# Optimization experiments

Measured on AMD Instinct MI355X. Metric: run time of the kernel, lower is better.

Reference implementation:

```python
import jax, jax.numpy as jnp
import numpy as np

B, T1, T2, D, H = 16, 512, 64, 768, 12
E = D // H  # head dim


def _proj(x, W, b):
    # x: [B,T,D], W: [6,D,D], b: [6,D] -> [6,B,H,T,E], scaled by E**-0.25 (applied to q,k,v alike, per source)
    t = x.shape[1]
    p = jnp.einsum('btd,kdf->kbtf', x, W) + b[:, None, None, :]
    p = p.reshape(6, B, t, H, E).transpose(0, 1, 3, 2, 4)
    return p * (E ** -0.25)


def setup_inputs() -> dict:
    key = jax.random.key(0)
    ks = jax.random.split(key, 12)
    s = 0.02
    return {
        'feats': jax.random.normal(ks[0], (B, T1, D), jnp.float32),
        'inps': jax.random.normal(ks[1], (B, T2, D), jnp.float32),
        'att_mask': jax.random.randint(ks[2], (B, 1, 1, T1 + T2), 0, 2).astype(bool),
        'W_f': s * jax.random.normal(ks[3], (6, D, D), jnp.float32),
        'b_f': s * jax.random.normal(ks[4], (6, D), jnp.float32),
        'W_i': s * jax.random.normal(ks[5], (6, D, D), jnp.float32),
        'b_i': s * jax.random.normal(ks[6], (6, D), jnp.float32),
        'Wu_v': s * jax.random.normal(ks[7], (D, D), jnp.float32),
        'bu_v': s * jax.random.normal(ks[8], (D,), jnp.float32),
        'Wu_l': s * jax.random.normal(ks[9], (D, D), jnp.float32),
        'bu_l': s * jax.random.normal(ks[10], (D,), jnp.float32),
    }


def reference(feats, inps, att_mask, W_f, b_f, W_i, b_i, Wu_v, bu_v, Wu_l, bu_l):
    NEG = jnp.float32(-1e9)
    # projections from feats: [keys_v_v, queries_v_v, values_v_v, queries_l_v, keys_v_l, values_v_l]
    k_vv, q_vv, v_vv, q_lv, k_vl, v_vl = _proj(feats, W_f, b_f)
    # projections from inps: [keys_l_v, values_l_v, queries_v_l, queries_l_l, keys_l_l, values_l_l]
    k_lv, v_lv, q_vl, q_ll, k_ll, v_ll = _proj(inps, W_i, b_i)

    # visual stream: two distinct queries over the two key blocks, joint softmax over t1+t2
    dot_vv = jnp.einsum('bhqe,bhke->bhqk', q_vv, k_vv)   # [B,H,T1,T1]
    dot_lv = jnp.einsum('bhqe,bhke->bhqk', q_lv, k_lv)   # [B,H,T1,T2]
    att_v = jnp.concatenate([dot_vv, dot_lv], axis=-1)    # [B,H,T1,T1+T2]
    att_v = jax.nn.softmax(jnp.where(att_mask, NEG, att_v), axis=-1)
    vals_v = jnp.concatenate([v_vv, v_lv], axis=2)        # [B,H,T1+T2,E]
    out_v = jnp.einsum('bhqk,bhke->bhqe', att_v, vals_v)
    out_v = out_v.transpose(0, 2, 1, 3).reshape(B, T1, D)
    out_v = out_v @ Wu_v + bu_v

    # language stream
    dot_vl = jnp.einsum('bhqe,bhke->bhqk', q_vl, k_vl)    # [B,H,T2,T1]
    dot_ll = jnp.einsum('bhqe,bhke->bhqk', q_ll, k_ll)    # [B,H,T2,T2]
    att_l = jnp.concatenate([dot_vl, dot_ll], axis=-1)    # [B,H,T2,T1+T2]
    att_l = jax.nn.softmax(jnp.where(att_mask, NEG, att_l), axis=-1)
    vals_l = jnp.concatenate([v_vl, v_ll], axis=2)        # [B,H,T1+T2,E]
    out_l = jnp.einsum('bhqk,bhke->bhqe', att_l, vals_l)
    out_l = out_l.transpose(0, 2, 1, 3).reshape(B, T2, D)
    out_l = out_l @ Wu_l + bu_l

    return (out_v, out_l)
```

## Files before the change

### kernel.cpp

```cpp
#include <hip/hip_runtime.h>
#include <stdint.h>

#define BB 16
#define T1C 512
#define T2C 64
#define DC 768
#define HC 12
#define EC 64
#define SC 576
#define QSCALE 0.35355339059327379f

typedef __attribute__((ext_vector_type(8))) short bf16x8;
typedef __attribute__((ext_vector_type(4))) float f32x4;

__device__ __forceinline__ uint16_t f2b(float f) {
    union { float f; uint32_t i; } v; v.f = f;
    return (uint16_t)((v.i + 0x7fffu + ((v.i >> 16) & 1u)) >> 16);
}
__device__ __forceinline__ uint16_t f2bfast(float f) {
    union { float f; uint32_t i; } v; v.f = f;
    return (uint16_t)((v.i + 0x8000u) >> 16);
}
__device__ __forceinline__ uint32_t pk2(float a, float b) {
    return (uint32_t)f2b(a) | ((uint32_t)f2b(b) << 16);
}

__device__ __forceinline__ void gll16(const void* g, void* l) {
    __builtin_amdgcn_global_load_lds(
        (const __attribute__((address_space(1))) uint32_t*)(uintptr_t)g,
        (__attribute__((address_space(3))) uint32_t*)(uintptr_t)l, 16, 0, 0);
}

#define WT_BLOCKS (24 * 24 * 14)
#define XS_BLOCKS 3456

__global__ __launch_bounds__(256) void prep(
    const float* __restrict__ Wf, const float* __restrict__ Wi,
    const float* __restrict__ Wuv, const float* __restrict__ Wul,
    uint16_t* __restrict__ Wt,
    const float* __restrict__ Xf, const float* __restrict__ Xi,
    uint16_t* __restrict__ Of, uint16_t* __restrict__ Oi,
    const uint32_t* __restrict__ mw, int* __restrict__ flags)
{
    __shared__ union { float tile[32][33]; int d[3]; } sh;
    const int bid = blockIdx.x;
    if (bid < WT_BLOCKS) {
        const int z = bid / 576, r = bid % 576;
        const int kx = r % 24, fy = r / 24;
        const float* src = (z < 6)  ? Wf + (size_t)z * DC * DC
                         : (z < 12) ? Wi + (size_t)(z - 6) * DC * DC
                         : (z == 12 ? Wuv : Wul);
        uint16_t* dst = Wt + (size_t)z * DC * DC;
        const int tx = threadIdx.x & 31, ty = threadIdx.x >> 5;
        const int k0 = kx * 32, f0 = fy * 32;
#pragma unroll
        for (int q = 0; q < 4; q++)
            sh.tile[ty + q * 8][tx] = src[(size_t)(k0 + ty + q * 8) * DC + f0 + tx];
        __syncthreads();
#pragma unroll
        for (int q = 0; q < 4; q++)
            dst[(size_t)(f0 + ty + q * 8) * DC + k0 + tx] = f2b(sh.tile[tx][ty + q * 8]);
    } else if (bid < WT_BLOCKS + XS_BLOCKS) {
        const int nf = BB * T1C * DC / 8;
        const int ni = BB * T2C * DC / 8;
        int t = (bid - WT_BLOCKS) * 256 + threadIdx.x;
        const float* src; uint16_t* dst; int cc;
        if (t < nf) { src = Xf; dst = Of; cc = t; }
        else        { cc = t - nf; if (cc >= ni) return; src = Xi; dst = Oi; }
        int rlid = cc & 15;
        int t2 = cc >> 4;
        int qd = t2 & 3;
        int t3 = t2 >> 2;
        int kt = t3 % 24;
        int p  = t3 / 24;
        const float* sp = src + (size_t)(p * 16 + rlid) * DC + kt * 32 + qd * 8;
        float4 a = *(const float4*)sp;
        float4 b = *(const float4*)(sp + 4);
        uint4 o;
        o.x = pk2(a.x, a.y); o.y = pk2(a.z, a.w);
        o.z = pk2(b.x, b.y); o.w = pk2(b.z, b.w);
        *(uint4*)(dst + (size_t)cc * 8) = o;
    } else {
        if (threadIdx.x == 0) { sh.d[0] = 0; sh.d[1] = 0; sh.d[2] = 0; }
        __syncthreads();
        int lW = 0, lB = 0, lL = 0;
        for (int i = threadIdx.x; i < 2304; i += 256) {
            uint32_t w = mw[i];
            if (w > 1u) lW = 1;
            if (((w) & 0xffu) > 1u || ((w >> 8) & 0xffu) > 1u ||
                ((w >> 16) & 0xffu) > 1u || ((w >> 24) & 0xffu) > 1u) lB = 1;
            if ((w & 0xffffu) > 1u) lL = 1;
        }
        if (lW) atomicOr(&sh.d[0], 1);
        if (lB) atomicOr(&sh.d[1], 1);
        if (lL) atomicOr(&sh.d[2], 1);
        __syncthreads();
        if (threadIdx.x == 0)
            flags[0] = (!sh.d[0]) ? 0 : ((!sh.d[1]) ? 1 : (sh.d[2] ? 2 : 0));
    }
}

#define BSTR 76

__global__ __launch_bounds__(256, 3) void gemm_proj_mfma(
    const uint16_t* __restrict__ Xsf, const uint16_t* __restrict__ Xsi,
    const uint16_t* __restrict__ Wt,
    const float* __restrict__ b_f, const float* __restrict__ b_i,
    uint16_t* __restrict__ Pf, uint16_t* __restrict__ Pi)
{
    __shared__ union {
        uint16_t B[2][128 * 32];
        uint16_t bounce[4][16 * BSTR];
    } sm;
    const int tid = threadIdx.x;
    const int w = tid >> 6, l = tid & 63;
    const bool isf = (blockIdx.x < 64);
    const int mx = isf ? blockIdx.x : blockIdx.x - 64;
    const int m0 = mx * 128;
    const int T  = isf ? T1C : T2C;
    const uint16_t* Xs = isf ? Xsf : Xsi;
    const float* bias  = isf ? b_f : b_i;
    uint16_t* P        = isf ? Pf : Pi;
    const int vmask    = isf ? 0x24 : 0x22;
    const int k6 = blockIdx.y / 6, nt = blockIdx.y % 6;
    const int n0 = nt * 128;
    const uint16_t* Bsrc = Wt + (size_t)((isf ? 0 : 6) + k6) * DC * DC;

    const int lid = l & 15, qd = l >> 4;
    const int wm = w >> 1, wn = w & 1;
    const int br = l >> 2, bk = (l & 3) * 8;
    const int p0 = mx * 8 + wm * 4;
    const int c0 = w * 2;

    f32x4 acc[4][4] = {};
    bf16x8 af0[4], af1[4];

#define PJ_A(dst, t) { _Pragma("unroll") for (int i = 0; i < 4; i++) \
        dst[i] = *(const bf16x8*)(Xs + ((size_t)((p0 + i) * 24 + (t)) * 64 + l) * 8); }
#define PJ_S(bu, t) { _Pragma("unroll") for (int n = 0; n < 2; n++) \
        gll16(Bsrc + (size_t)(n0 + (c0 + n) * 16 + br) * DC + (t) * 32 + bk, \
              &sm.B[bu][(c0 + n) * 512]); }
#define PJ_C(bu, afc) { bf16x8 bq[4]; \
        _Pragma("unroll") for (int j = 0; j < 4; j++) \
            bq[j] = *(const bf16x8*)&sm.B[bu][(wn * 64 + j * 16 + lid) * 32 + qd * 8]; \
        _Pragma("unroll") for (int i = 0; i < 4; i++) \
        _Pragma("unroll") for (int j = 0; j < 4; j++) \
            acc[i][j] = __builtin_amdgcn_mfma_f32_16x16x32_bf16(afc[i], bq[j], acc[i][j], 0, 0, 0); }

    PJ_A(af0, 0);
    PJ_S(0, 0);

    for (int k2 = 0; k2 < 12; ++k2) {
        PJ_A(af1, 2 * k2 + 1);
        __builtin_amdgcn_s_barrier();
        __builtin_amdgcn_sched_barrier(0);
        PJ_S(1, 2 * k2 + 1);
        asm volatile("s_waitcnt vmcnt(6)" ::: "memory");
        __builtin_amdgcn_sched_barrier(0);
        __builtin_amdgcn_s_barrier();
        __builtin_amdgcn_sched_barrier(0);
        PJ_C(0, af0);
        if (k2 < 11) { PJ_A(af0, 2 * k2 + 2); }
        __builtin_amdgcn_s_barrier();
        __builtin_amdgcn_sched_barrier(0);
        if (k2 < 11) {
            PJ_S(0, 2 * k2 + 2);
            asm volatile("s_waitcnt vmcnt(6)" ::: "memory");
        } else {
            asm volatile("s_waitcnt vmcnt(0)" ::: "memory");
        }
        __builtin_amdgcn_sched_barrier(0);
        __builtin_amdgcn_s_barrier();
        __builtin_amdgcn_sched_barrier(0);
        PJ_C(1, af1);
    }
#undef PJ_A
#undef PJ_S
#undef PJ_C

    float bv[4];
#pragma unroll
    for (int j = 0; j < 4; j++)
        bv[j] = bias[k6 * DC + n0 + wn * 64 + j * 16 + lid];
    __syncthreads();

    uint16_t* reg = sm.bounce[w];
    const int mb = m0 + wm * 64;
    const int b = mb / T, tb = mb - b * T;
    const int h = nt * 2 + wn;
    const int rrow = l >> 2;
    const int rcol = (l & 3) * 16;

    if (!((vmask >> k6) & 1)) {
        uint16_t* dst0 = P + ((((size_t)k6 * BB + b) * HC + h) * T + tb + rrow) * EC + rcol;
#pragma unroll
        for (int p = 0; p < 4; p++) {
#pragma unroll
            for (int j = 0; j < 4; j++)
#pragma unroll
                for (int r = 0; r < 4; r++)
                    reg[(qd * 4 + r) * BSTR + j * 16 + lid] =
                        f2b((acc[p][j][r] + bv[j]) * QSCALE);
            uint4 d0 = *(const uint4*)&reg[rrow * BSTR + rcol];
            uint4 d1 = *(const uint4*)&reg[rrow * BSTR + rcol + 8];
            uint16_t* dst = dst0 + (size_t)p * 16 * EC;
            *(uint4*)dst = d0;
            *(uint4*)(dst + 8) = d1;
        }
    } else {
        uint16_t* dst0 = P + (size_t)k6 * BB * HC * T * EC
                           + (((size_t)b * HC + h) * EC + rrow) * T + tb + rcol;
#pragma unroll
        for (int p = 0; p < 4; p++) {
#pragma unroll
            for (int i = 0; i < 4; i++) {
                uint32_t w0 = pk2((acc[i][p][0] + bv[p]) * QSCALE,
                                  (acc[i][p][1] + bv[p]) * QSCALE);
                uint32_t w1 = pk2((acc[i][p][2] + bv[p]) * QSCALE,
                                  (acc[i][p][3] + bv[p]) * QSCALE);
                *(uint2*)&reg[lid * BSTR + i * 16 + qd * 4] = make_uint2(w0, w1);
            }
            uint4 d0 = *(const uint4*)&reg[rrow * BSTR + rcol];
            uint4 d1 = *(const uint4*)&reg[rrow * BSTR + rcol + 8];
            uint16_t* dst = dst0 + (size_t)p * 16 * T;
            *(uint4*)dst = d0;
            *(uint4*)(dst + 8) = d1;
        }
    }
}

__global__ __launch_bounds__(256, 3) void gemm_out_mfma(
    const uint16_t* __restrict__ Osv, const uint16_t* __restrict__ Osl,
    const uint16_t* __restrict__ Wt,
    const float* __restrict__ bu_v, const float* __restrict__ bu_l,
    float* __restrict__ out)
{
    __shared__ uint16_t Bs[2][128 * 32];
    const int tid = threadIdx.x;
    const int w = tid >> 6, l = tid & 63;
    const bool isv = (blockIdx.x < 64);
    const int mx = isv ? blockIdx.x : blockIdx.x - 64;
    const int m0 = mx * 128;
    const int rowoff = isv ? 0 : BB * T1C;
    const uint16_t* A = isv ? Osv : Osl;
    const uint16_t* Wtm = Wt + (size_t)(isv ? 12 : 13) * DC * DC;
    const float* bias = isv ? bu_v : bu_l;
    const int n0 = blockIdx.y * 128;
    const int lid = l & 15, qd = l >> 4;
    const int wm = w >> 1, wn = w & 1;
    const int br = l >> 2, bk = (l & 3) * 8;
    const int p0 = mx * 8 + wm * 4;
    const int c0 = w * 2;

    f32x4 acc[4][4] = {};
    bf16x8 af0[4], af1[4];

#define GO_A(dst, t) { _Pragma("unroll") for (int i = 0; i < 4; i++) \
        dst[i] = *(const bf16x8*)(A + ((size_t)((p0 + i) * 24 + (t)) * 64 + l) * 8); }
#define GO_S(bu, t) { _Pragma("unroll") for (int n = 0; n < 2; n++) \
        gll16(Wtm + (size_t)(n0 + (c0 + n) * 16 + br) * DC + (t) * 32 + bk, \
              &Bs[bu][(c0 + n) * 512]); }
#define GO_C(bu, afc) { bf16x8 bq[4]; \
        _Pragma("unroll") for (int j = 0; j < 4; j++) \
            bq[j] = *(const bf16x8*)&Bs[bu][(wn * 64 + j * 16 + lid) * 32 + qd * 8]; \
        _Pragma("unroll") for (int i = 0; i < 4; i++) \
        _Pragma("unroll") for (int j = 0; j < 4; j++) \
            acc[i][j] = __builtin_amdgcn_mfma_f32_16x16x32_bf16(afc[i], bq[j], acc[i][j], 0, 0, 0); }

    GO_A(af0, 0);
    GO_S(0, 0);

    for (int k2 = 0; k2 < 12; ++k2) {
        GO_A(af1, 2 * k2 + 1);
        __builtin_amdgcn_s_barrier();
        __builtin_amdgcn_sched_barrier(0);
        GO_S(1, 2 * k2 + 1);
        asm volatile("s_waitcnt vmcnt(6)" ::: "memory");
        __builtin_amdgcn_sched_barrier(0);
        __builtin_amdgcn_s_barrier();
        __builtin_amdgcn_sched_barrier(0);
        GO_C(0, af0);
        if (k2 < 11) { GO_A(af0, 2 * k2 + 2); }
        __builtin_amdgcn_s_barrier();
        __builtin_amdgcn_sched_barrier(0);
        if (k2 < 11) {
            GO_S(0, 2 * k2 + 2);
            asm volatile("s_waitcnt vmcnt(6)" ::: "memory");
        } else {
            asm volatile("s_waitcnt vmcnt(0)" ::: "memory");
        }
        __builtin_amdgcn_sched_barrier(0);
        __builtin_amdgcn_s_barrier();
        __builtin_amdgcn_sched_barrier(0);
        GO_C(1, af1);
    }
#undef GO_A
#undef GO_S
#undef GO_C

    float bv[4];
#pragma unroll
    for (int j = 0; j < 4; j++)
        bv[j] = bias[n0 + wn * 64 + j * 16 + lid];
#pragma unroll
    for (int i = 0; i < 4; i++)
#pragma unroll
        for (int j = 0; j < 4; j++)
#pragma unroll
            for (int r = 0; r < 4; r++) {
                int m = m0 + wm * 64 + i * 16 + qd * 4 + r;
                int f = n0 + wn * 64 + j * 16 + lid;
                out[(size_t)(rowoff + m) * DC + f] = acc[i][j][r] + bv[j];
            }
}

__global__ __launch_bounds__(256, 3) void attn_mfma(
    const uint16_t* __restrict__ Pf,
    const uint16_t* __restrict__ Pi,
    const void* __restrict__ maskp,
    const int* __restrict__ flags,
    uint16_t* __restrict__ Osv,
    uint16_t* __restrict__ Osl)
{
    __shared__ uint16_t Klds[64 * 72];
    __shared__ uint16_t Vlds[64 * 72];
    __shared__ uint16_t Plds[4][16 * 72];
    __shared__ float    Ma[SC];
    __shared__ float    Lw[4][16];

    const int bh = blockIdx.x;
    const int tile = blockIdx.y;
    const int b = bh / HC, h = bh % HC;
    const int tid = threadIdx.x;
    const int w = tid >> 6, l = tid & 63;
    const int lid = l & 15, qd = l >> 4;

    const size_t SF = (size_t)BB * HC * T1C * EC;
    const size_t SI = (size_t)BB * HC * T2C * EC;

    const bool vis = (tile < 8);
    const uint16_t *Qa, *Qb, *K1, *K2, *V1, *V2;
    uint16_t* O; int Tq, q0;
    if (vis) { Qa = Pf + 1 * SF; Qb = Pf + 3 * SF; K1 = Pf;          K2 = Pi;
               V1 = Pf + 2 * SF; V2 = Pi + 1 * SI; O = Osv; Tq = T1C; q0 = tile * 64; }
    else     { Qa = Pi + 2 * SI; Qb = Pi + 3 * SI; K1 = Pf + 4 * SF; K2 = Pi + 4 * SI;
               V1 = Pf + 5 * SF; V2 = Pi + 5 * SI; O = Osl; Tq = T2C; q0 = 0; }

    {
        const int kind = flags[0];
        for (int i = tid; i < SC; i += 256) {
            int idx = b * SC + i;
            int mv;
            if (kind == 0)      mv = ((const uint32_t*)maskp)[idx] != 0u;
            else if (kind == 1) mv = ((const uint8_t*)maskp)[idx] != 0;
            else                mv = ((const uint16_t*)maskp)[idx] != 0;
            Ma[i] = mv ? -1e9f : 0.0f;
        }
    }

    const int q = q0 + w * 16 + lid;
    const uint16_t* Qrow  = Qa + ((size_t)bh * Tq + q) * EC;
    const uint16_t* Qrow2 = Qb + ((size_t)bh * Tq + q) * EC;
    bf16x8 qf0 = *(const bf16x8*)(Qrow + qd * 8);
    bf16x8 qf1 = *(const bf16x8*)(Qrow + 32 + qd * 8);
    bf16x8 qg0 = *(const bf16x8*)(Qrow2 + qd * 8);
    bf16x8 qg1 = *(const bf16x8*)(Qrow2 + 32 + qd * 8);

    f32x4 o[4];
#pragma unroll
    for (int ef = 0; ef < 4; ef++) { o[ef][0]=0.f; o[ef][1]=0.f; o[ef][2]=0.f; o[ef][3]=0.f; }
    float u[4] = {0.f, 0.f, 0.f, 0.f};

    const int skey = tid >> 2, se0 = (tid & 3) * 16;
    const int ve = tid >> 2,  vc = tid & 3;

    auto kptr = [&](int c) -> const uint16_t* {
        return (c < 8) ? K1 + ((size_t)bh * T1C + c * 64 + skey) * EC + se0
                       : K2 + ((size_t)bh * T2C + skey) * EC + se0;
    };
    auto vptr = [&](int c) -> const uint16_t* {
        return (c < 8) ? V1 + ((size_t)bh * EC + ve) * T1C + c * 64 + vc * 16
                       : V2 + ((size_t)bh * EC + ve) * T2C + vc * 16;
    };

    uint4 ka0 = *(const uint4*)kptr(0);
    uint4 ka1 = *(const uint4*)(kptr(0) + 8);
    uint4 va0 = *(const uint4*)vptr(0);
    uint4 va1 = *(const uint4*)(vptr(0) + 8);

#pragma unroll
    for (int c = 0; c < 9; ++c) {
        uint4 kb0, kb1, vb0, vb1;
        if (c < 8) {
            kb0 = *(const uint4*)kptr(c + 1);
            kb1 = *(const uint4*)(kptr(c + 1) + 8);
            vb0 = *(const uint4*)vptr(c + 1);
            vb1 = *(const uint4*)(vptr(c + 1) + 8);
        }
        __builtin_amdgcn_s_barrier();
        __builtin_amdgcn_sched_barrier(0);
        *(uint4*)&Klds[skey * 72 + se0]         = ka0;
        *(uint4*)&Klds[skey * 72 + se0 + 8]     = ka1;
        *(uint4*)&Vlds[ve * 72 + vc * 16]       = va0;
        *(uint4*)&Vlds[ve * 72 + vc * 16 + 8]   = va1;
        asm volatile("s_waitcnt lgkmcnt(0)" ::: "memory");
        __builtin_amdgcn_sched_barrier(0);
        __builtin_amdgcn_s_barrier();
        __builtin_amdgcn_sched_barrier(0);

        const int k0 = c * 64;
        const bf16x8 q_0 = (c < 8) ? qf0 : qg0;
        const bf16x8 q_1 = (c < 8) ? qf1 : qg1;
        f32x4 s[4];
#pragma unroll
        for (int sub = 0; sub < 4; sub++) {
            bf16x8 kf0 = *(const bf16x8*)&Klds[(sub * 16 + lid) * 72 + qd * 8];
            bf16x8 kf1 = *(const bf16x8*)&Klds[(sub * 16 + lid) * 72 + 32 + qd * 8];
            f32x4 z; z[0]=0.f; z[1]=0.f; z[2]=0.f; z[3]=0.f;
            z = __builtin_amdgcn_mfma_f32_16x16x32_bf16(q_0, kf0, z, 0, 0, 0);
            s[sub] = __builtin_amdgcn_mfma_f32_16x16x32_bf16(q_1, kf1, z, 0, 0, 0);
        }
#pragma unroll
        for (int sub = 0; sub < 4; sub++) {
            float mv = Ma[k0 + sub * 16 + lid];
#pragma unroll
            for (int r = 0; r < 4; r++) {
                float p = __expf(s[sub][r] + mv);
                u[r] += p;
                Plds[w][(qd * 4 + r) * 72 + sub * 16 + lid] = f2bfast(p);
            }
        }
#pragma unroll
        for (int half = 0; half < 2; half++) {
            bf16x8 pf = *(const bf16x8*)&Plds[w][lid * 72 + half * 32 + qd * 8];
#pragma unroll
            for (int ef = 0; ef < 4; ef++) {
                bf16x8 vf = *(const bf16x8*)&Vlds[(ef * 16 + lid) * 72 + half * 32 + qd * 8];
                o[ef] = __builtin_amdgcn_mfma_f32_16x16x32_bf16(vf, pf, o[ef], 0, 0, 0);
            }
        }
        if (c < 8) { ka0 = kb0; ka1 = kb1; va0 = vb0; va1 = vb1; }
    }

#pragma unroll
    for (int d = 1; d <= 8; d <<= 1)
#pragma unroll
        for (int r = 0; r < 4; r++)
            u[r] += __shfl_xor(u[r], d, 64);
    if (lid == 0) {
#pragma unroll
        for (int r = 0; r < 4; r++) Lw[w][qd * 4 + r] = u[r];
    }
    float rl = 1.f / Lw[w][lid];

    const size_t p = ((size_t)b * Tq + q0 + w * 16) >> 4;
#pragma unroll
    for (int ef = 0; ef < 4; ef++) {
        uint32_t w0 = pk2(o[ef][0] * rl, o[ef][1] * rl);
        uint32_t w1 = pk2(o[ef][2] * rl, o[ef][3] * rl);
        size_t chunk = ((p * 24 + h * 2 + (ef >> 1)) * 4 + (ef & 1) * 2 + (qd >> 1)) * 16 + lid;
        *(uint2*)(O + chunk * 8 + (qd & 1) * 4) = make_uint2(w0, w1);
    }
}

extern "C" void kernel_launch(void* const* d_in, const int* in_sizes, int n_in,
                              void* d_out, int out_size, void* d_ws, size_t ws_size,
                              hipStream_t stream)
{
    const float* feats = (const float*)d_in[0];
    const float* inps  = (const float*)d_in[1];
    const void*  maskp = d_in[2];
    const float* W_f   = (const float*)d_in[3];
    const float* b_f   = (const float*)d_in[4];
    const float* W_i   = (const float*)d_in[5];
    const float* b_i   = (const float*)d_in[6];
    const float* Wu_v  = (const float*)d_in[7];
    const float* bu_v  = (const float*)d_in[8];
    const float* Wu_l  = (const float*)d_in[9];
    const float* bu_l  = (const float*)d_in[10];

    const size_t MAT = (size_t)DC * DC;
    const size_t PF_E = 6ull * BB * HC * T1C * EC;
    const size_t PI_E = 6ull * BB * HC * T2C * EC;
    uint16_t* Wt  = (uint16_t*)d_ws;
    uint16_t* Osv = Wt;
    uint16_t* Osl = Wt + (size_t)BB * T1C * HC * EC;
    uint16_t* Pf  = Wt + 14 * MAT;
    uint16_t* Pi  = Pf + PF_E;
    int* flags    = (int*)(Pi + PI_E);

    uint16_t* Xsf = (uint16_t*)d_out;
    uint16_t* Xsi = Xsf + (size_t)BB * T1C * DC;

    prep<<<dim3(WT_BLOCKS + XS_BLOCKS + 1), dim3(256), 0, stream>>>(
        W_f, W_i, Wu_v, Wu_l, Wt, feats, inps, Xsf, Xsi,
        (const uint32_t*)maskp, flags);

    gemm_proj_mfma<<<dim3(72, 36), dim3(256), 0, stream>>>(
        Xsf, Xsi, Wt, b_f, b_i, Pf, Pi);

    attn_mfma<<<dim3(BB * HC, 9), dim3(256), 0, stream>>>(
        Pf, Pi, maskp, flags, Osv, Osl);

    gemm_out_mfma<<<dim3(72, 6), dim3(256), 0, stream>>>(
        Osv, Osl, Wt, bu_v, bu_l, (float*)d_out);
}
```

Measured before the change: 257.1 us.

## Stage A tiles through LDS via direct loads in projection and output GEMMs

Both GEMM kernels now load the activation (A) tiles into double-buffered LDS with global-to-LDS loads, next to the weight tiles, instead of having each wave load A fragments straight from global memory into registers. Each A tile is fetched once per block and shared by the two waves that use it, which cuts duplicate global traffic and drops the af0/af1 register buffers. The unrolled two-step loop becomes a simple 24-step loop, and launch bounds move from 3 to 4 blocks per CU to raise occupancy. In exchange, LDS use doubles to 32 KB per block, and each step adds LDS reads for A, which may add bank conflicts or barrier stalls.

```diff
diff --git a/kernel.cpp b/kernel.cpp
--- a/kernel.cpp
+++ b/kernel.cpp
@@ -102,14 +102,14 @@
 
 #define BSTR 76
 
-__global__ __launch_bounds__(256, 3) void gemm_proj_mfma(
+__global__ __launch_bounds__(256, 4) void gemm_proj_mfma(
     const uint16_t* __restrict__ Xsf, const uint16_t* __restrict__ Xsi,
     const uint16_t* __restrict__ Wt,
     const float* __restrict__ b_f, const float* __restrict__ b_i,
     uint16_t* __restrict__ Pf, uint16_t* __restrict__ Pi)
 {
     __shared__ union {
-        uint16_t B[2][128 * 32];
+        struct { uint16_t A[2][128 * 32]; uint16_t B[2][128 * 32]; } st;
         uint16_t bounce[4][16 * BSTR];
     } sm;
     const int tid = threadIdx.x;
@@ -129,52 +129,43 @@
     const int lid = l & 15, qd = l >> 4;
     const int wm = w >> 1, wn = w & 1;
     const int br = l >> 2, bk = (l & 3) * 8;
-    const int p0 = mx * 8 + wm * 4;
     const int c0 = w * 2;
 
     f32x4 acc[4][4] = {};
-    bf16x8 af0[4], af1[4];
-
-#define PJ_A(dst, t) { _Pragma("unroll") for (int i = 0; i < 4; i++) \
-        dst[i] = *(const bf16x8*)(Xs + ((size_t)((p0 + i) * 24 + (t)) * 64 + l) * 8); }
-#define PJ_S(bu, t) { _Pragma("unroll") for (int n = 0; n < 2; n++) \
-        gll16(Bsrc + (size_t)(n0 + (c0 + n) * 16 + br) * DC + (t) * 32 + bk, \
-              &sm.B[bu][(c0 + n) * 512]); }
-#define PJ_C(bu, afc) { bf16x8 bq[4]; \
+
+#define PJ_S(bu, t) { \
+        _Pragma("unroll") for (int n = 0; n < 2; n++) \
+            gll16(Xs + ((size_t)((mx * 8 + c0 + n) * 24 + (t)) * 64 + l) * 8, \
+                  &sm.st.A[bu][(c0 + n) * 512]); \
+        _Pragma("unroll") for (int n = 0; n < 2; n++) \
+            gll16(Bsrc + (size_t)(n0 + (c0 + n) * 16 + br) * DC + (t) * 32 + bk, \
+                  &sm.st.B[bu][(c0 + n) * 512]); }
+#define PJ_C(bu) { bf16x8 aq[4], bq[4]; \
+        _Pragma("unroll") for (int i = 0; i < 4; i++) \
+            aq[i] = *(const bf16x8*)&sm.st.A[bu][((wm * 4 + i) * 64 + l) * 8]; \
         _Pragma("unroll") for (int j = 0; j < 4; j++) \
-            bq[j] = *(const bf16x8*)&sm.B[bu][(wn * 64 + j * 16 + lid) * 32 + qd * 8]; \
+            bq[j] = *(const bf16x8*)&sm.st.B[bu][(wn * 64 + j * 16 + lid) * 32 + qd * 8]; \
         _Pragma("unroll") for (int i = 0; i < 4; i++) \
         _Pragma("unroll") for (int j = 0; j < 4; j++) \
-            acc[i][j] = __builtin_amdgcn_mfma_f32_16x16x32_bf16(afc[i], bq[j], acc[i][j], 0, 0, 0); }
-
-    PJ_A(af0, 0);
+            acc[i][j] = __builtin_amdgcn_mfma_f32_16x16x32_bf16(aq[i], bq[j], acc[i][j], 0, 0, 0); }
+
     PJ_S(0, 0);
 
-    for (int k2 = 0; k2 < 12; ++k2) {
-        PJ_A(af1, 2 * k2 + 1);
-        __builtin_amdgcn_s_barrier();
-        __builtin_amdgcn_sched_barrier(0);
-        PJ_S(1, 2 * k2 + 1);
-        asm volatile("s_waitcnt vmcnt(6)" ::: "memory");
-        __builtin_amdgcn_sched_barrier(0);
-        __builtin_amdgcn_s_barrier();
-        __builtin_amdgcn_sched_barrier(0);
-        PJ_C(0, af0);
-        if (k2 < 11) { PJ_A(af0, 2 * k2 + 2); }
-        __builtin_amdgcn_s_barrier();
-        __builtin_amdgcn_sched_barrier(0);
-        if (k2 < 11) {
-            PJ_S(0, 2 * k2 + 2);
-            asm volatile("s_waitcnt vmcnt(6)" ::: "memory");
+    for (int kt = 0; kt < DC / 32; ++kt) {
+        const int cb = kt & 1, nb = cb ^ 1;
+        __builtin_amdgcn_s_barrier();
+        __builtin_amdgcn_sched_barrier(0);
+        if (kt < 23) {
+            PJ_S(nb, kt + 1);
+            asm volatile("s_waitcnt vmcnt(4)" ::: "memory");
         } else {
             asm volatile("s_waitcnt vmcnt(0)" ::: "memory");
         }
         __builtin_amdgcn_sched_barrier(0);
         __builtin_amdgcn_s_barrier();
         __builtin_amdgcn_sched_barrier(0);
-        PJ_C(1, af1);
-    }
-#undef PJ_A
+        PJ_C(cb);
+    }
 #undef PJ_S
 #undef PJ_C
 
@@ -229,13 +220,13 @@
     }
 }
 
-__global__ __launch_bounds__(256, 3) void gemm_out_mfma(
+__global__ __launch_bounds__(256, 4) void gemm_out_mfma(
     const uint16_t* __restrict__ Osv, const uint16_t* __restrict__ Osl,
     const uint16_t* __restrict__ Wt,
     const float* __restrict__ bu_v, const float* __restrict__ bu_l,
     float* __restrict__ out)
 {
-    __shared__ uint16_t Bs[2][128 * 32];
+    __shared__ struct { uint16_t A[2][128 * 32]; uint16_t B[2][128 * 32]; } st;
     const int tid = threadIdx.x;
     const int w = tid >> 6, l = tid & 63;
     const bool isv = (blockIdx.x < 64);
@@ -249,52 +240,43 @@
     const int lid = l & 15, qd = l >> 4;
     const int wm = w >> 1, wn = w & 1;
     const int br = l >> 2, bk = (l & 3) * 8;
-    const int p0 = mx * 8 + wm * 4;
     const int c0 = w * 2;
 
     f32x4 acc[4][4] = {};
-    bf16x8 af0[4], af1[4];
-
-#define GO_A(dst, t) { _Pragma("unroll") for (int i = 0; i < 4; i++) \
-        dst[i] = *(const bf16x8*)(A + ((size_t)((p0 + i) * 24 + (t)) * 64 + l) * 8); }
-#define GO_S(bu, t) { _Pragma("unroll") for (int n = 0; n < 2; n++) \
-        gll16(Wtm + (size_t)(n0 + (c0 + n) * 16 + br) * DC + (t) * 32 + bk, \
-              &Bs[bu][(c0 + n) * 512]); }
-#define GO_C(bu, afc) { bf16x8 bq[4]; \
+
+#define GO_S(bu, t) { \
+        _Pragma("unroll") for (int n = 0; n < 2; n++) \
+            gll16(A + ((size_t)((mx * 8 + c0 + n) * 24 + (t)) * 64 + l) * 8, \
+                  &st.A[bu][(c0 + n) * 512]); \
+        _Pragma("unroll") for (int n = 0; n < 2; n++) \
+            gll16(Wtm + (size_t)(n0 + (c0 + n) * 16 + br) * DC + (t) * 32 + bk, \
+                  &st.B[bu][(c0 + n) * 512]); }
+#define GO_C(bu) { bf16x8 aq[4], bq[4]; \
+        _Pragma("unroll") for (int i = 0; i < 4; i++) \
+            aq[i] = *(const bf16x8*)&st.A[bu][((wm * 4 + i) * 64 + l) * 8]; \
         _Pragma("unroll") for (int j = 0; j < 4; j++) \
-            bq[j] = *(const bf16x8*)&Bs[bu][(wn * 64 + j * 16 + lid) * 32 + qd * 8]; \
+            bq[j] = *(const bf16x8*)&st.B[bu][(wn * 64 + j * 16 + lid) * 32 + qd * 8]; \
         _Pragma("unroll") for (int i = 0; i < 4; i++) \
         _Pragma("unroll") for (int j = 0; j < 4; j++) \
-            acc[i][j] = __builtin_amdgcn_mfma_f32_16x16x32_bf16(afc[i], bq[j], acc[i][j], 0, 0, 0); }
-
-    GO_A(af0, 0);
+            acc[i][j] = __builtin_amdgcn_mfma_f32_16x16x32_bf16(aq[i], bq[j], acc[i][j], 0, 0, 0); }
+
     GO_S(0, 0);
 
-    for (int k2 = 0; k2 < 12; ++k2) {
-        GO_A(af1, 2 * k2 + 1);
-        __builtin_amdgcn_s_barrier();
-        __builtin_amdgcn_sched_barrier(0);
-        GO_S(1, 2 * k2 + 1);
-        asm volatile("s_waitcnt vmcnt(6)" ::: "memory");
-        __builtin_amdgcn_sched_barrier(0);
-        __builtin_amdgcn_s_barrier();
-        __builtin_amdgcn_sched_barrier(0);
-        GO_C(0, af0);
-        if (k2 < 11) { GO_A(af0, 2 * k2 + 2); }
-        __builtin_amdgcn_s_barrier();
-        __builtin_amdgcn_sched_barrier(0);
-        if (k2 < 11) {
-            GO_S(0, 2 * k2 + 2);
-            asm volatile("s_waitcnt vmcnt(6)" ::: "memory");
+    for (int kt = 0; kt < DC / 32; ++kt) {
+        const int cb = kt & 1, nb = cb ^ 1;
+        __builtin_amdgcn_s_barrier();
+        __builtin_amdgcn_sched_barrier(0);
+        if (kt < 23) {
+            GO_S(nb, kt + 1);
+            asm volatile("s_waitcnt vmcnt(4)" ::: "memory");
         } else {
             asm volatile("s_waitcnt vmcnt(0)" ::: "memory");
         }
         __builtin_amdgcn_sched_barrier(0);
         __builtin_amdgcn_s_barrier();
         __builtin_amdgcn_sched_barrier(0);
-        GO_C(1, af1);
-    }
-#undef GO_A
+        GO_C(cb);
+    }
 #undef GO_S
 #undef GO_C
 
```

Result: no change. 254.9 us (-0.8%).
